# Optimization experiments

Measured on AMD Instinct MI355X. Metric: run time of the kernel, lower is better.

Reference implementation:

```python
import jax, jax.numpy as jnp
import numpy as np

VOCAB, B, T, E, H, C = 50000, 1024, 120, 50, 300, 5
FORGET_BIAS = 1.0  # tf.nn.rnn_cell.LSTMCell default


def setup_inputs() -> dict:
    key = jax.random.key(0)
    ks = jax.random.split(key, 8)
    tokens = jax.random.randint(ks[0], (B, T, 1), 0, VOCAB, dtype=jnp.int32)
    labels = jax.random.randint(ks[1], (B, T), 0, C, dtype=jnp.int32)
    mask = jax.random.randint(ks[2], (B, T), 0, 2, dtype=jnp.int32).astype(bool)
    embeddings = jax.random.normal(ks[3], (VOCAB, E), dtype=jnp.float32) * 0.1
    Wx = jax.random.normal(ks[4], (E, 4 * H), dtype=jnp.float32) * (1.0 / np.sqrt(E))
    Wh = jax.random.normal(ks[5], (H, 4 * H), dtype=jnp.float32) * (1.0 / np.sqrt(H))
    b = jnp.zeros((4 * H,), dtype=jnp.float32)
    U = jax.random.normal(ks[6], (H, C), dtype=jnp.float32) * (1.0 / np.sqrt(H))
    b2 = jnp.zeros((C,), dtype=jnp.float32)
    return {"tokens": tokens, "labels": labels, "mask": mask,
            "embeddings": embeddings, "Wx": Wx, "Wh": Wh, "b": b, "U": U, "b2": b2}


def reference(tokens, labels, mask, embeddings, Wx, Wh, b, U, b2):
    # Embedding lookup: (B, T, n_features=1) -> (B, T, E)
    x = embeddings[tokens[..., 0]]

    def step(carry, xt):
        c, h = carry
        z = xt @ Wx + h @ Wh + b           # (B, 4H), gate order i, j, f, o
        i, j, f, o = jnp.split(z, 4, axis=-1)
        c_new = jax.nn.sigmoid(f + FORGET_BIAS) * c + jax.nn.sigmoid(i) * jnp.tanh(j)
        h_new = jax.nn.sigmoid(o) * jnp.tanh(c_new)
        return (c_new, h_new), h_new

    nb = x.shape[0]
    c0 = jnp.zeros((nb, H), dtype=x.dtype)
    h0 = jnp.zeros((nb, H), dtype=x.dtype)
    _, hs = jax.lax.scan(step, (c0, h0), jnp.swapaxes(x, 0, 1))  # (T, B, H)
    hs = jnp.swapaxes(hs, 0, 1)                                   # (B, T, H)

    logits = hs @ U + b2                                          # (B, T, C)
    logp = jax.nn.log_softmax(logits, axis=-1)
    ce = -jnp.take_along_axis(logp, labels[..., None].astype(jnp.int32), axis=-1)[..., 0]
    m = mask.astype(ce.dtype)
    loss = jnp.sum(ce * m) / jnp.sum(m)  # mean over unmasked tokens
    return loss
```

## Files before the change

kernel.cpp:

```cpp
#include <hip/hip_runtime.h>
#include <hip/hip_bf16.h>
#include <math.h>

#define NBATCH 1024
#define NT 120
#define NE 50
#define NH 300
#define NC 5
#define GH 1200
#define NKPAD 352
#define NSTRIP 15
#define HS 20
#define SCOL 80
#define NGRP 16
#define BB 64
#define ASTR 376
#define WSTR 376
#define ZSTR 84
#define HBSTR 304
#define HCH 76
#define NCHUNK 4800

typedef __attribute__((ext_vector_type(8))) short short8;
typedef __attribute__((ext_vector_type(4))) float f32x4;
typedef __attribute__((ext_vector_type(2))) unsigned short us2;

static __device__ __forceinline__ float bf2f(unsigned short u) {
    unsigned int x = ((unsigned int)u) << 16;
    return __builtin_bit_cast(float, x);
}
static __device__ __forceinline__ unsigned short f2bf(float f) {
    __hip_bfloat16 h = __float2bfloat16(f);
    return __builtin_bit_cast(unsigned short, h);
}

static __device__ __forceinline__ float sigmoid_fast(float x) {
    return __builtin_amdgcn_rcpf(1.f + __expf(-x));
}
static __device__ __forceinline__ float tanh_fast(float x) {
    return 1.f - 2.f * __builtin_amdgcn_rcpf(1.f + __expf(2.f * x));
}

__global__ __launch_bounds__(256)
void wswz_kernel(const float* __restrict__ Wx, const float* __restrict__ Wh,
                 unsigned short* __restrict__ Wswz)
{
    int idx = blockIdx.x * 256 + threadIdx.x;
    if (idx >= NSTRIP * SCOL * NKPAD) return;
    int s = idx / (SCOL * NKPAD);
    int r = idx % (SCOL * NKPAD);
    int j = r / NKPAD, k = r % NKPAD;
    int col = (j & 3) * NH + s * HS + (j >> 2);
    float v = 0.f;
    if (k < NH)           v = Wh[k * GH + col];
    else if (k < NH + NE) v = Wx[(k - NH) * GH + col];
    Wswz[idx] = f2bf(v);
}

__device__ __forceinline__ void load_h(const unsigned short* __restrict__ hb,
                                       int b0, unsigned short* A_s, int tid)
{
    const unsigned long long* src =
        (const unsigned long long*)(hb + (size_t)b0 * HBSTR);
    unsigned long long v[19];
#pragma unroll
    for (int m = 0; m < 19; ++m) {
        const int idx = tid + 256 * m;
        if (idx < NCHUNK) {
            const int row = idx / 75, j = idx % 75;
            v[m] = __hip_atomic_load(src + (size_t)row * HCH + j,
                                     __ATOMIC_RELAXED, __HIP_MEMORY_SCOPE_AGENT);
        }
    }
#pragma unroll
    for (int m = 0; m < 19; ++m) {
        const int idx = tid + 256 * m;
        if (idx < NCHUNK) {
            const int row = idx / 75, j = idx % 75;
            *(unsigned long long*)(A_s + row * ASTR + j * 4) = v[m];
        }
    }
}

__device__ __forceinline__ void store_h(unsigned short* hb, int b0, int st,
                                        const unsigned short* h_stage, int tid)
{
#pragma unroll
    for (int m = 0; m < 2; ++m) {
        const int c = tid + m * 256;
        if (c < 320) {
            const int row = c / 5, j = c % 5;
            unsigned long long val =
                *(const unsigned long long*)(h_stage + row * HS + j * 4);
            unsigned long long* p = (unsigned long long*)
                (hb + (size_t)(b0 + row) * HBSTR + st * HS + j * 4);
            __hip_atomic_store(p, val, __ATOMIC_RELAXED,
                               __HIP_MEMORY_SCOPE_AGENT);
        }
    }
}

__device__ __forceinline__ void load_x(const int* __restrict__ tokens,
                                       const float* __restrict__ emb,
                                       int b0, int t, unsigned short* A_s, int tid)
{
    const int row = tid >> 2, q = tid & 3;
    const int tok = tokens[(b0 + row) * NT + t];
    const float* er = emb + (size_t)tok * NE;
    unsigned short* dst = A_s + row * ASTR + NH;
    for (int m = 0; m < 7; ++m) {
        int f = q + 4 * m;
        if (f < 25) {
            float2 v = *(const float2*)(er + f * 2);
            us2 o; o.x = f2bf(v.x); o.y = f2bf(v.y);
            *(us2*)(dst + f * 2) = o;
        }
    }
}

__device__ __forceinline__ void do_ce(bool doCE, int tc, int b0, int r0, int nr,
        const unsigned short* A_s, const float* U_s, const float* __restrict__ b2,
        const int* __restrict__ labels, const int* __restrict__ mask,
        float* __restrict__ ce_arr, float* llds, float* lgl, int tid)
{
    if (doCE && tid < nr * 50) {
        int i = tid / 50, rem = tid % 50, c = rem / 10, q = rem % 10;
        const unsigned short* ar = A_s + (r0 + i) * ASTR + q * 30;
        const float* up = U_s + q * 30 * NC + c;
        float acc = 0.f;
#pragma unroll
        for (int k = 0; k < 30; ++k) acc += bf2f(ar[k]) * up[k * NC];
        llds[i * 50 + c * 10 + q] = acc;
    }
    __syncthreads();
    if (doCE && tid < nr * NC) {
        int i = tid / NC, c = tid % NC;
        const float* pp = llds + i * 50 + c * 10;
        float sum = pp[0]+pp[1]+pp[2]+pp[3]+pp[4]+pp[5]+pp[6]+pp[7]+pp[8]+pp[9];
        lgl[i * NC + c] = sum + b2[c];
    }
    __syncthreads();
    if (doCE && tid < nr) {
        const float* L = lgl + tid * NC;
        float m = fmaxf(fmaxf(fmaxf(L[0], L[1]), fmaxf(L[2], L[3])), L[4]);
        float ssum = expf(L[0]-m)+expf(L[1]-m)+expf(L[2]-m)+expf(L[3]-m)+expf(L[4]-m);
        float lse = m + logf(ssum);
        int bidx = b0 + r0 + tid;
        int lab = labels[bidx * NT + tc];
        int mk  = mask[bidx * NT + tc];
        ce_arr[bidx * NT + tc] = mk ? (lse - L[lab]) : 0.f;
    }
}

__global__ __launch_bounds__(256, 1)
void lstm_persist(const int* __restrict__ tokens,
                  const int* __restrict__ labels,
                  const int* __restrict__ mask,
                  const float* __restrict__ emb,
                  const float* __restrict__ bias,
                  const float* __restrict__ U,
                  const float* __restrict__ b2,
                  const unsigned short* __restrict__ Wswz,
                  unsigned short* __restrict__ hbuf,
                  float* __restrict__ ce_arr,
                  int* __restrict__ flags)
{
    __shared__ unsigned short A_s[BB * ASTR];
    __shared__ unsigned short W_s[SCOL * WSTR];
    __shared__ __align__(16) unsigned short h_stage[BB * HS];
    __shared__ float z_s[BB * ZSTR];
    __shared__ float c_s[BB * HS];
    __shared__ float U_s[NH * NC];
    __shared__ float b_s[SCOL];
    __shared__ float llds[5 * 50];
    __shared__ float lgl[32];

    const int tid  = threadIdx.x;
    const int g    = blockIdx.x & 15;
    const int s    = blockIdx.x >> 4;
    const int b0   = g * BB;
    const int wave = tid >> 6;
    const int lane = tid & 63;
    const int c15  = lane & 15;
    const int kq   = lane >> 4;
    const int r0   = (s * BB) / NSTRIP;
    const int r1   = ((s + 1) * BB) / NSTRIP;
    const int nr   = r1 - r0;

    for (int idx = tid; idx < SCOL * 44; idx += 256) {
        int j = idx / 44, ch = idx % 44;
        *(uint4*)(W_s + j * WSTR + ch * 8) =
            *(const uint4*)(Wswz + (size_t)s * SCOL * NKPAD + j * NKPAD + ch * 8);
    }
    for (int idx = tid; idx < BB * NH; idx += 256) {
        int row = idx / NH, k = idx % NH;
        A_s[row * ASTR + k] = 0;
    }
    for (int idx = tid; idx < BB * 26; idx += 256) {
        int row = idx / 26, k = 350 + idx % 26;
        A_s[row * ASTR + k] = 0;
    }
    for (int idx = tid; idx < BB * HS; idx += 256) c_s[idx] = 0.f;
    for (int idx = tid; idx < NH * NC; idx += 256) U_s[idx] = U[idx];
    if (tid < SCOL) b_s[tid] = bias[(tid & 3) * NH + s * HS + (tid >> 2)];
    load_x(tokens, emb, b0, 0, A_s, tid);
    __syncthreads();

    const unsigned short* Ab = A_s + (wave * 16 + c15) * ASTR + kq * 8;
    const unsigned short* Wb = W_s + c15 * WSTR + kq * 8;

    for (int t = 0; t < NT; ++t) {
        f32x4 acc[5];
#pragma unroll
        for (int n = 0; n < 5; ++n) acc[n] = (f32x4){0.f, 0.f, 0.f, 0.f};
#pragma unroll
        for (int ks = 0; ks < 11; ++ks) {
            short8 av = *(const short8*)(Ab + ks * 32);
#pragma unroll
            for (int n = 0; n < 5; ++n) {
                short8 bv = *(const short8*)(Wb + n * 16 * WSTR + ks * 32);
                acc[n] = __builtin_amdgcn_mfma_f32_16x16x32_bf16(av, bv, acc[n], 0, 0, 0);
            }
        }
#pragma unroll
        for (int n = 0; n < 5; ++n)
#pragma unroll
            for (int j = 0; j < 4; ++j)
                z_s[(wave * 16 + kq * 4 + j) * ZSTR + n * 16 + c15] = acc[n][j];
        __syncthreads();

        if (t + 1 < NT) load_x(tokens, emb, b0, t + 1, A_s, tid);
#pragma unroll
        for (int ii = 0; ii < 5; ++ii) {
            int idx = tid * 5 + ii;
            int row = idx / HS, h = idx % HS;
            f32x4 z4 = *(f32x4*)(z_s + row * ZSTR + h * 4);
            float zi = z4[0] + b_s[4 * h + 0];
            float zj = z4[1] + b_s[4 * h + 1];
            float zf = z4[2] + b_s[4 * h + 2];
            float zo = z4[3] + b_s[4 * h + 3];
            float co = c_s[idx];
            float fg = sigmoid_fast(zf + 1.f);
            float ig = sigmoid_fast(zi);
            float og = sigmoid_fast(zo);
            float cn = fg * co + ig * tanh_fast(zj);
            float hn = og * tanh_fast(cn);
            c_s[idx] = cn;
            h_stage[idx] = f2bf(hn);
        }
        __syncthreads();

        unsigned short* hb = hbuf + (size_t)(t & 1) * (NBATCH * HBSTR);
        store_h(hb, b0, s, h_stage, tid);
        asm volatile("s_waitcnt vmcnt(0)" ::: "memory");
        __syncthreads();

        if (tid == 0)
            __hip_atomic_store(flags + (size_t)(t * NGRP + g) * 16 + s, 1,
                               __ATOMIC_RELAXED, __HIP_MEMORY_SCOPE_AGENT);

        do_ce(t >= 1, t - 1, b0, r0, nr, A_s, U_s, b2, labels, mask,
              ce_arr, llds, lgl, tid);

        if (tid < NSTRIP) {
            const int* fp = flags + (size_t)(t * NGRP + g) * 16 + tid;
            int fv = 0; int gu = 0;
            do {
                fv = __hip_atomic_load(fp, __ATOMIC_RELAXED,
                                       __HIP_MEMORY_SCOPE_AGENT);
                if (!fv) __builtin_amdgcn_s_sleep(1);
            } while (!fv && ++gu < (1 << 17));
        }
        __syncthreads();

        load_h(hb, b0, A_s, tid);
        __syncthreads();
    }

    do_ce(true, NT - 1, b0, r0, nr, A_s, U_s, b2, labels, mask,
          ce_arr, llds, lgl, tid);
}

__global__ __launch_bounds__(256)
void reduce1_kernel(const float* __restrict__ ce_arr,
                    const int* __restrict__ mask,
                    float* __restrict__ pce, float* __restrict__ pm)
{
    __shared__ float s_ce[256];
    __shared__ float s_m[256];
    const int tid = threadIdx.x;
    const int lo = blockIdx.x * 480;
    float ac = 0.f, am = 0.f;
    for (int i = lo + tid; i < lo + 480; i += 256) {
        ac += ce_arr[i];
        am += (float)mask[i];
    }
    s_ce[tid] = ac; s_m[tid] = am;
    __syncthreads();
    for (int r = 128; r > 0; r >>= 1) {
        if (tid < r) { s_ce[tid] += s_ce[tid + r]; s_m[tid] += s_m[tid + r]; }
        __syncthreads();
    }
    if (tid == 0) { pce[blockIdx.x] = s_ce[0]; pm[blockIdx.x] = s_m[0]; }
}

__global__ __launch_bounds__(256)
void reduce2_kernel(const float* __restrict__ pce,
                    const float* __restrict__ pm,
                    float* __restrict__ out)
{
    __shared__ float s_ce[256];
    __shared__ float s_m[256];
    const int tid = threadIdx.x;
    s_ce[tid] = pce[tid];
    s_m[tid]  = pm[tid];
    __syncthreads();
    for (int r = 128; r > 0; r >>= 1) {
        if (tid < r) { s_ce[tid] += s_ce[tid + r]; s_m[tid] += s_m[tid + r]; }
        __syncthreads();
    }
    if (tid == 0) out[0] = s_ce[0] / s_m[0];
}

extern "C" void kernel_launch(void* const* d_in, const int* in_sizes, int n_in,
                              void* d_out, int out_size, void* d_ws, size_t ws_size,
                              hipStream_t stream)
{
    const int*   tokens = (const int*)d_in[0];
    const int*   labels = (const int*)d_in[1];
    const int*   mask   = (const int*)d_in[2];
    const float* emb    = (const float*)d_in[3];
    const float* Wx     = (const float*)d_in[4];
    const float* Wh     = (const float*)d_in[5];
    const float* bias   = (const float*)d_in[6];
    const float* U      = (const float*)d_in[7];
    const float* b2     = (const float*)d_in[8];

    char* wsb = (char*)d_ws;
    unsigned short* Wswz = (unsigned short*)wsb;
    unsigned short* hbuf = (unsigned short*)(wsb + 844800);
    float* ce    = (float*)(wsb + 2089984);
    float* pce   = (float*)(wsb + 2581504);
    float* pm    = (float*)(wsb + 2582528);
    int*   flags = (int*)(wsb + 2583552);

    hipMemsetAsync(flags, 0, 122880, stream);
    wswz_kernel<<<(NSTRIP * SCOL * NKPAD + 255) / 256, 256, 0, stream>>>(Wx, Wh, Wswz);
    lstm_persist<<<NGRP * NSTRIP, 256, 0, stream>>>(
        tokens, labels, mask, emb, bias, U, b2, Wswz, hbuf, ce, flags);
    reduce1_kernel<<<256, 256, 0, stream>>>(ce, mask, pce, pm);
    reduce2_kernel<<<1, 256, 0, stream>>>(pce, pm, (float*)d_out);
}
```

Before: 643.8 us.

## Overlap CE logits with h store and flag polling, cut per-step barriers

The per-step cross-entropy work is split in two. The partial logit dot products now run right after the hidden-state store is issued, before the vmcnt wait, so they overlap the global store. The final reduction and softmax run on waves 0-2 while wave 3 polls the inter-block flags, which removes two __syncthreads per timestep and the lgl buffer. The risk is that the busy waves lengthen the critical path before the flag wait, and that lane reuse across waves creates imbalance.

```diff
diff --git a/kernel.cpp b/kernel.cpp
--- a/kernel.cpp
+++ b/kernel.cpp
@@ -118,13 +118,12 @@
     }
 }
 
-__device__ __forceinline__ void do_ce(bool doCE, int tc, int b0, int r0, int nr,
-        const unsigned short* A_s, const float* U_s, const float* __restrict__ b2,
-        const int* __restrict__ labels, const int* __restrict__ mask,
-        float* __restrict__ ce_arr, float* llds, float* lgl, int tid)
-{
-    if (doCE && tid < nr * 50) {
-        int i = tid / 50, rem = tid % 50, c = rem / 10, q = rem % 10;
+__device__ __forceinline__ void ce_phase0(bool doCE, int r0, int nr,
+        const unsigned short* A_s, const float* U_s, float* llds, int tid)
+{
+    if (!doCE || tid >= 192) return;
+    for (int item = tid; item < nr * 50; item += 192) {
+        int i = item / 50, rem = item % 50, c = rem / 10, q = rem % 10;
         const unsigned short* ar = A_s + (r0 + i) * ASTR + q * 30;
         const float* up = U_s + q * 30 * NC + c;
         float acc = 0.f;
@@ -132,24 +131,30 @@
         for (int k = 0; k < 30; ++k) acc += bf2f(ar[k]) * up[k * NC];
         llds[i * 50 + c * 10 + q] = acc;
     }
-    __syncthreads();
-    if (doCE && tid < nr * NC) {
-        int i = tid / NC, c = tid % NC;
-        const float* pp = llds + i * 50 + c * 10;
-        float sum = pp[0]+pp[1]+pp[2]+pp[3]+pp[4]+pp[5]+pp[6]+pp[7]+pp[8]+pp[9];
-        lgl[i * NC + c] = sum + b2[c];
-    }
-    __syncthreads();
-    if (doCE && tid < nr) {
-        const float* L = lgl + tid * NC;
-        float m = fmaxf(fmaxf(fmaxf(L[0], L[1]), fmaxf(L[2], L[3])), L[4]);
-        float ssum = expf(L[0]-m)+expf(L[1]-m)+expf(L[2]-m)+expf(L[3]-m)+expf(L[4]-m);
-        float lse = m + logf(ssum);
-        int bidx = b0 + r0 + tid;
-        int lab = labels[bidx * NT + tc];
-        int mk  = mask[bidx * NT + tc];
-        ce_arr[bidx * NT + tc] = mk ? (lse - L[lab]) : 0.f;
-    }
+}
+
+__device__ __forceinline__ void ce_final(bool doCE, int tc, int b0, int r0,
+        int nr, const float* b2r, const int* __restrict__ labels,
+        const int* __restrict__ mask, float* __restrict__ ce_arr,
+        const float* llds, int tid)
+{
+    if (!doCE || tid >= nr) return;
+    const float* pp = llds + tid * 50;
+    float L[5];
+#pragma unroll
+    for (int c = 0; c < 5; ++c) {
+        float sum = 0.f;
+#pragma unroll
+        for (int q = 0; q < 10; ++q) sum += pp[c * 10 + q];
+        L[c] = sum + b2r[c];
+    }
+    float m = fmaxf(fmaxf(fmaxf(L[0], L[1]), fmaxf(L[2], L[3])), L[4]);
+    float ssum = expf(L[0]-m)+expf(L[1]-m)+expf(L[2]-m)+expf(L[3]-m)+expf(L[4]-m);
+    float lse = m + logf(ssum);
+    int bidx = b0 + r0 + tid;
+    int lab = labels[bidx * NT + tc];
+    int mk  = mask[bidx * NT + tc];
+    ce_arr[bidx * NT + tc] = mk ? (lse - L[lab]) : 0.f;
 }
 
 __global__ __launch_bounds__(256, 1)
@@ -173,7 +178,6 @@
     __shared__ float U_s[NH * NC];
     __shared__ float b_s[SCOL];
     __shared__ float llds[5 * 50];
-    __shared__ float lgl[32];
 
     const int tid  = threadIdx.x;
     const int g    = blockIdx.x & 15;
@@ -203,6 +207,9 @@
     for (int idx = tid; idx < BB * HS; idx += 256) c_s[idx] = 0.f;
     for (int idx = tid; idx < NH * NC; idx += 256) U_s[idx] = U[idx];
     if (tid < SCOL) b_s[tid] = bias[(tid & 3) * NH + s * HS + (tid >> 2)];
+    float b2r[5];
+#pragma unroll
+    for (int c = 0; c < 5; ++c) b2r[c] = b2[c];
     load_x(tokens, emb, b0, 0, A_s, tid);
     __syncthreads();
 
@@ -252,24 +259,26 @@
 
         unsigned short* hb = hbuf + (size_t)(t & 1) * (NBATCH * HBSTR);
         store_h(hb, b0, s, h_stage, tid);
+        ce_phase0(t >= 1, r0, nr, A_s, U_s, llds, tid);
         asm volatile("s_waitcnt vmcnt(0)" ::: "memory");
         __syncthreads();
 
         if (tid == 0)
             __hip_atomic_store(flags + (size_t)(t * NGRP + g) * 16 + s, 1,
                                __ATOMIC_RELAXED, __HIP_MEMORY_SCOPE_AGENT);
-
-        do_ce(t >= 1, t - 1, b0, r0, nr, A_s, U_s, b2, labels, mask,
-              ce_arr, llds, lgl, tid);
-
-        if (tid < NSTRIP) {
-            const int* fp = flags + (size_t)(t * NGRP + g) * 16 + tid;
-            int fv = 0; int gu = 0;
-            do {
-                fv = __hip_atomic_load(fp, __ATOMIC_RELAXED,
-                                       __HIP_MEMORY_SCOPE_AGENT);
-                if (!fv) __builtin_amdgcn_s_sleep(1);
-            } while (!fv && ++gu < (1 << 17));
+        if (tid >= 192) {
+            if (tid < 192 + NSTRIP) {
+                const int* fp = flags + (size_t)(t * NGRP + g) * 16 + (tid - 192);
+                int fv = 0; int gu = 0;
+                do {
+                    fv = __hip_atomic_load(fp, __ATOMIC_RELAXED,
+                                           __HIP_MEMORY_SCOPE_AGENT);
+                    if (!fv) __builtin_amdgcn_s_sleep(1);
+                } while (!fv && ++gu < (1 << 17));
+            }
+        } else {
+            ce_final(t >= 1, t - 1, b0, r0, nr, b2r, labels, mask,
+                     ce_arr, llds, tid);
         }
         __syncthreads();
 
@@ -277,8 +286,9 @@
         __syncthreads();
     }
 
-    do_ce(true, NT - 1, b0, r0, nr, A_s, U_s, b2, labels, mask,
-          ce_arr, llds, lgl, tid);
+    ce_phase0(true, r0, nr, A_s, U_s, llds, tid);
+    __syncthreads();
+    ce_final(true, NT - 1, b0, r0, nr, b2r, labels, mask, ce_arr, llds, tid);
 }
 
 __global__ __launch_bounds__(256)
```

After: 670.1 us. +4.1%, slower.
